# Kernel optimization log

Hardware: AMD Instinct MI355X
Metric: run time of the kernel (lower is better)

Reference implementation:

```python
import jax, jax.numpy as jnp
import numpy as np


def setup_inputs() -> dict:
    key = jax.random.key(0)
    k1, k2, k3, k4 = jax.random.split(key, 4)
    B, n, f, k = 32768, 512, 30, 40
    X = jax.random.normal(k1, (B, n), dtype=jnp.float32)
    w1 = jax.random.normal(k2, (n, 1), dtype=jnp.float32) * 0.01
    b = jnp.zeros((1,), dtype=jnp.float32)
    v = jax.random.normal(k3, (n, f, k), dtype=jnp.float32) * 0.01
    feature2field = jax.random.randint(k4, (n,), 0, f, dtype=jnp.int32)
    return {"X": X, "w1": w1, "b": b, "v": v, "feature2field": feature2field}


def reference(X, w1, b, v, feature2field):
    # linear terms: [B]
    linear = (X @ w1).reshape(-1) + b[0]
    n = v.shape[0]
    # A[i, j] = v[i, feature2field[j]]  -> [n, n, k]
    A = v[:, feature2field, :]
    # pair coefficient C[i, j] = sum_k v[i, field[j], k] * v[j, field[i], k]
    C = jnp.einsum('ijk,jik->ij', A, A)
    # strict upper triangle matches the i<j loop in the original
    Cm = C * jnp.triu(jnp.ones((n, n), dtype=C.dtype), k=1)
    # interaction[b] = sum_{i<j} C[i,j] * X[b,i] * X[b,j]
    inter = jnp.einsum('bi,ij,bj->b', X, Cm, X)
    logits = linear + inter
    return jax.nn.sigmoid(logits)
```

## Files before the change

### kernel.cpp

```cpp
#include <hip/hip_runtime.h>
#include <hip/hip_bf16.h>
#include <math.h>


#define N_FEAT 512
#define FK 1200
#define KDIM 40
#define B_ROWS 32768
#define BM 128
#define BN 128
#define BK 64

typedef __attribute__((ext_vector_type(8))) short short8;
typedef __attribute__((ext_vector_type(4))) float f32x4;

__device__ __forceinline__ unsigned short bf16_rne(float f) {
    union { float f; unsigned int u; } c; c.f = f;
    unsigned int u = c.u;
    u += 0x7fffu + ((u >> 16) & 1u);
    return (unsigned short)(u >> 16);
}

__device__ __forceinline__ void async_copy16(const void* g, void* l) {
    __builtin_amdgcn_global_load_lds(
        (const __attribute__((address_space(1))) void*)g,
        (__attribute__((address_space(3))) void*)l,
        16, 0, 0);
}

__global__ __launch_bounds__(256) void cvt_x(const float* __restrict__ X,
                                             unsigned short* __restrict__ Xb) {
    const int i = blockIdx.x * 256 + threadIdx.x;
    f32x4 x = ((const f32x4*)X)[i];
    ushort4 o;
    o.x = bf16_rne(x.x);
    o.y = bf16_rne(x.y);
    o.z = bf16_rne(x.z);
    o.w = bf16_rne(x.w);
    ((ushort4*)Xb)[i] = o;
}

__global__ __launch_bounds__(256) void build_w16(const float* __restrict__ v,
                                                 const int* __restrict__ f2f,
                                                 unsigned short* __restrict__ W16) {
    const int j = blockIdx.x * 256 + threadIdx.x;
    const int i = blockIdx.y;
    const int fi = f2f[i];
    const int fj = f2f[j];
    const float4* a = (const float4*)(v + (size_t)i * FK + (size_t)fj * KDIM);
    const float4* c = (const float4*)(v + (size_t)j * FK + (size_t)fi * KDIM);
    float acc = 0.f;
#pragma unroll
    for (int q = 0; q < KDIM / 4; ++q) {
        float4 av = a[q], cv = c[q];
        acc = fmaf(av.x, cv.x, acc);
        acc = fmaf(av.y, cv.y, acc);
        acc = fmaf(av.z, cv.z, acc);
        acc = fmaf(av.w, cv.w, acc);
    }
    W16[(size_t)i * N_FEAT + j] = (i == j) ? (unsigned short)0 : bf16_rne(0.5f * acc);
}

__global__ __launch_bounds__(256) void ffm_mfma(const unsigned short* __restrict__ Xb,
                                                const unsigned short* __restrict__ W16,
                                                const float* __restrict__ X,
                                                const float* __restrict__ w1,
                                                float* __restrict__ pOut) {
    __shared__ unsigned short As[BM * BK];
    __shared__ unsigned short Bs[BN * BK];
    __shared__ float part[2][BM];

    const int tid  = threadIdx.x;
    const int lane = tid & 63;
    const int wave = tid >> 6;
    const int wm = wave & 1;
    const int wn = wave >> 1;
    const int quad = lane >> 4;
    const int l16  = lane & 15;

    const int cb   = blockIdx.x;
    const int col0 = cb * BN;
    const size_t row0 = (size_t)blockIdx.y * BM;

    f32x4 acc[4][4];
#pragma unroll
    for (int mi = 0; mi < 4; ++mi)
#pragma unroll
        for (int ni = 0; ni < 4; ++ni)
            acc[mi][ni] = (f32x4){0.f, 0.f, 0.f, 0.f};

    const int srow = lane >> 3;
    const int scol = (((lane & 7) ^ (srow & 7)) * 8);

    const int aswz = l16 & 7;

    for (int k0 = 0; k0 < N_FEAT; k0 += BK) {
#pragma unroll
        for (int c = 0; c < 4; ++c) {
            const int chunk = wave * 4 + c;
            const int r = chunk * 8 + srow;
            async_copy16(Xb  + (row0 + r) * N_FEAT + k0 + scol, As + chunk * 512);
            async_copy16(W16 + (size_t)(col0 + r) * N_FEAT + k0 + scol, Bs + chunk * 512);
        }
        __syncthreads();

#pragma unroll
        for (int kk = 0; kk < 2; ++kk) {
            short8 a[4], b[4];
            const int kc = kk * 4 + quad;
            const int swc = (kc ^ aswz) * 8;
#pragma unroll
            for (int mi = 0; mi < 4; ++mi) {
                const int ar = wm * 64 + mi * 16 + l16;
                a[mi] = *(const short8*)(As + ar * BK + swc);
            }
#pragma unroll
            for (int ni = 0; ni < 4; ++ni) {
                const int br = wn * 64 + ni * 16 + l16;
                b[ni] = *(const short8*)(Bs + br * BK + swc);
            }
#pragma unroll
            for (int mi = 0; mi < 4; ++mi)
#pragma unroll
                for (int ni = 0; ni < 4; ++ni)
                    acc[mi][ni] = __builtin_amdgcn_mfma_f32_16x16x32_bf16(
                        a[mi], b[ni], acc[mi][ni], 0, 0, 0);
        }
        __syncthreads();
    }

#pragma unroll
    for (int mi = 0; mi < 4; ++mi) {
        float rs[4] = {0.f, 0.f, 0.f, 0.f};
        const size_t growb = row0 + wm * 64 + mi * 16 + quad * 4;
#pragma unroll
        for (int ni = 0; ni < 4; ++ni) {
            const int gcol = col0 + wn * 64 + ni * 16 + l16;
            const float w1v = w1[gcol];
#pragma unroll
            for (int reg = 0; reg < 4; ++reg) {
                const float xv = X[(growb + reg) * N_FEAT + gcol];
                rs[reg] += xv * (acc[mi][ni][reg] + w1v);
            }
        }
#pragma unroll
        for (int off = 1; off < 16; off <<= 1)
#pragma unroll
            for (int reg = 0; reg < 4; ++reg)
                rs[reg] += __shfl_xor(rs[reg], off, 16);
        if (l16 == 0) {
            const int lrow = wm * 64 + mi * 16 + quad * 4;
#pragma unroll
            for (int reg = 0; reg < 4; ++reg)
                part[wn][lrow + reg] = rs[reg];
        }
    }
    __syncthreads();

    if (tid < BM) {
        pOut[(size_t)cb * B_ROWS + row0 + tid] = part[0][tid] + part[1][tid];
    }
}

__global__ __launch_bounds__(256) void ffm_final(const float* __restrict__ p,
                                                 const float* __restrict__ bvec,
                                                 float* __restrict__ out) {
    const int i = blockIdx.x * 256 + threadIdx.x;
    const float t = p[i] + p[B_ROWS + i] + p[2 * B_ROWS + i] + p[3 * B_ROWS + i] + bvec[0];
    out[i] = 1.0f / (1.0f + expf(-t));
}

extern "C" void kernel_launch(void* const* d_in, const int* in_sizes, int n_in,
                              void* d_out, int out_size, void* d_ws, size_t ws_size,
                              hipStream_t stream) {
    const float* X   = (const float*)d_in[0];
    const float* w1  = (const float*)d_in[1];
    const float* b   = (const float*)d_in[2];
    const float* v   = (const float*)d_in[3];
    const int*   f2f = (const int*)d_in[4];
    float* out = (float*)d_out;

    unsigned short* W16 = (unsigned short*)d_ws;
    unsigned short* Xb  = (unsigned short*)((char*)d_ws + (1u << 20));
    float*          pP  = (float*)((char*)d_ws + (1u << 20) + (32u << 20));

    cvt_x<<<(B_ROWS * N_FEAT / 4) / 256, 256, 0, stream>>>(X, Xb);
    build_w16<<<dim3(2, N_FEAT), 256, 0, stream>>>(v, f2f, W16);
    ffm_mfma<<<dim3(4, B_ROWS / BM), 256, 0, stream>>>(Xb, W16, X, w1, pP);
    ffm_final<<<B_ROWS / 256, 256, 0, stream>>>(pP, b, out);
}
```

Before: 146.8 us.

## Fuse X conversion, GEMM over all columns, and sigmoid into one kernel

Removes the separate fp32-to-bf16 conversion kernel and the final reduction kernel. Each block now loads its 128 rows of X once, converts them to bf16 and keeps the full 128x512 tile resident in padded LDS. It then loops over all four column blocks of W, forms the X·(W+w1) row dot products in registers, and applies the sigmoid directly. This drops the Xb and partial-sum round trips through global memory and two launches. In exchange the grid shrinks to 256 blocks, and LDS use grows to about 150KB per block, capping occupancy at one block per CU. The epilogue also now uses bf16-rounded X instead of fp32 X, which adds a small accuracy change.

```diff
diff --git a/kernel.cpp b/kernel.cpp
--- a/kernel.cpp
+++ b/kernel.cpp
@@ -8,8 +8,8 @@
 #define KDIM 40
 #define B_ROWS 32768
 #define BM 128
-#define BN 128
 #define BK 64
+#define APAD 520
 
 typedef __attribute__((ext_vector_type(8))) short short8;
 typedef __attribute__((ext_vector_type(4))) float f32x4;
@@ -21,23 +21,17 @@
     return (unsigned short)(u >> 16);
 }
 
+__device__ __forceinline__ float bf16_to_f(unsigned short h) {
+    union { unsigned int u; float f; } c;
+    c.u = ((unsigned int)h) << 16;
+    return c.f;
+}
+
 __device__ __forceinline__ void async_copy16(const void* g, void* l) {
     __builtin_amdgcn_global_load_lds(
         (const __attribute__((address_space(1))) void*)g,
         (__attribute__((address_space(3))) void*)l,
         16, 0, 0);
-}
-
-__global__ __launch_bounds__(256) void cvt_x(const float* __restrict__ X,
-                                             unsigned short* __restrict__ Xb) {
-    const int i = blockIdx.x * 256 + threadIdx.x;
-    f32x4 x = ((const f32x4*)X)[i];
-    ushort4 o;
-    o.x = bf16_rne(x.x);
-    o.y = bf16_rne(x.y);
-    o.z = bf16_rne(x.z);
-    o.w = bf16_rne(x.w);
-    ((ushort4*)Xb)[i] = o;
 }
 
 __global__ __launch_bounds__(256) void build_w16(const float* __restrict__ v,
@@ -61,13 +55,13 @@
     W16[(size_t)i * N_FEAT + j] = (i == j) ? (unsigned short)0 : bf16_rne(0.5f * acc);
 }
 
-__global__ __launch_bounds__(256) void ffm_mfma(const unsigned short* __restrict__ Xb,
-                                                const unsigned short* __restrict__ W16,
-                                                const float* __restrict__ X,
-                                                const float* __restrict__ w1,
-                                                float* __restrict__ pOut) {
-    __shared__ unsigned short As[BM * BK];
-    __shared__ unsigned short Bs[BN * BK];
+__global__ __launch_bounds__(256, 1) void ffm_fused(const float* __restrict__ X,
+                                                    const unsigned short* __restrict__ W16,
+                                                    const float* __restrict__ w1,
+                                                    const float* __restrict__ bvec,
+                                                    float* __restrict__ out) {
+    __shared__ __align__(16) unsigned short As[BM * APAD];
+    __shared__ __align__(16) unsigned short Bs[128 * BK];
     __shared__ float part[2][BM];
 
     const int tid  = threadIdx.x;
@@ -78,96 +72,119 @@
     const int quad = lane >> 4;
     const int l16  = lane & 15;
 
-    const int cb   = blockIdx.x;
-    const int col0 = cb * BN;
-    const size_t row0 = (size_t)blockIdx.y * BM;
-
-    f32x4 acc[4][4];
+    const size_t row0 = (size_t)blockIdx.x * BM;
+
+    {
+        const float4* X4 = (const float4*)(X + row0 * N_FEAT);
+        for (int u = 0; u < 32; ++u) {
+            const int g  = u * 256 + tid;
+            const int r  = g >> 6;
+            const int cc = g & 63;
+            float4 f0 = X4[r * 128 + cc * 2];
+            float4 f1 = X4[r * 128 + cc * 2 + 1];
+            union { unsigned short us[8]; short8 v; } pk;
+            pk.us[0] = bf16_rne(f0.x);
+            pk.us[1] = bf16_rne(f0.y);
+            pk.us[2] = bf16_rne(f0.z);
+            pk.us[3] = bf16_rne(f0.w);
+            pk.us[4] = bf16_rne(f1.x);
+            pk.us[5] = bf16_rne(f1.y);
+            pk.us[6] = bf16_rne(f1.z);
+            pk.us[7] = bf16_rne(f1.w);
+            *(short8*)(As + r * APAD + cc * 8) = pk.v;
+        }
+    }
+
+    const int srow = lane >> 3;
+    const int scol = (((lane & 7) ^ srow) * 8);
+    const int aswz = l16 & 7;
+
+    float rs[4][4];
 #pragma unroll
     for (int mi = 0; mi < 4; ++mi)
 #pragma unroll
+        for (int reg = 0; reg < 4; ++reg) rs[mi][reg] = 0.f;
+
+    for (int cb = 0; cb < 4; ++cb) {
+        const int col0 = cb * 128;
+
+        f32x4 acc[4][4];
+#pragma unroll
+        for (int mi = 0; mi < 4; ++mi)
+#pragma unroll
+            for (int ni = 0; ni < 4; ++ni)
+                acc[mi][ni] = (f32x4){0.f, 0.f, 0.f, 0.f};
+
+        for (int k0 = 0; k0 < N_FEAT; k0 += BK) {
+            __syncthreads();
+#pragma unroll
+            for (int c = 0; c < 4; ++c) {
+                const int chunk = wave * 4 + c;
+                const int r = chunk * 8 + srow;
+                async_copy16(W16 + (size_t)(col0 + r) * N_FEAT + k0 + scol,
+                             Bs + chunk * 512);
+            }
+            __syncthreads();
+
+#pragma unroll
+            for (int kk = 0; kk < 2; ++kk) {
+                short8 a[4], b[4];
+#pragma unroll
+                for (int mi = 0; mi < 4; ++mi) {
+                    const int ar = wm * 64 + mi * 16 + l16;
+                    a[mi] = *(const short8*)(As + ar * APAD + k0 + kk * 32 + quad * 8);
+                }
+                const int swc = ((kk * 4 + quad) ^ aswz) * 8;
+#pragma unroll
+                for (int ni = 0; ni < 4; ++ni) {
+                    const int br = wn * 64 + ni * 16 + l16;
+                    b[ni] = *(const short8*)(Bs + br * BK + swc);
+                }
+#pragma unroll
+                for (int mi = 0; mi < 4; ++mi)
+#pragma unroll
+                    for (int ni = 0; ni < 4; ++ni)
+                        acc[mi][ni] = __builtin_amdgcn_mfma_f32_16x16x32_bf16(
+                            a[mi], b[ni], acc[mi][ni], 0, 0, 0);
+            }
+        }
+
+        float w1v[4];
+#pragma unroll
         for (int ni = 0; ni < 4; ++ni)
-            acc[mi][ni] = (f32x4){0.f, 0.f, 0.f, 0.f};
-
-    const int srow = lane >> 3;
-    const int scol = (((lane & 7) ^ (srow & 7)) * 8);
-
-    const int aswz = l16 & 7;
-
-    for (int k0 = 0; k0 < N_FEAT; k0 += BK) {
-#pragma unroll
-        for (int c = 0; c < 4; ++c) {
-            const int chunk = wave * 4 + c;
-            const int r = chunk * 8 + srow;
-            async_copy16(Xb  + (row0 + r) * N_FEAT + k0 + scol, As + chunk * 512);
-            async_copy16(W16 + (size_t)(col0 + r) * N_FEAT + k0 + scol, Bs + chunk * 512);
-        }
-        __syncthreads();
-
-#pragma unroll
-        for (int kk = 0; kk < 2; ++kk) {
-            short8 a[4], b[4];
-            const int kc = kk * 4 + quad;
-            const int swc = (kc ^ aswz) * 8;
-#pragma unroll
-            for (int mi = 0; mi < 4; ++mi) {
-                const int ar = wm * 64 + mi * 16 + l16;
-                a[mi] = *(const short8*)(As + ar * BK + swc);
+            w1v[ni] = w1[col0 + wn * 64 + ni * 16 + l16];
+#pragma unroll
+        for (int mi = 0; mi < 4; ++mi) {
+#pragma unroll
+            for (int ni = 0; ni < 4; ++ni) {
+                const int gc = col0 + wn * 64 + ni * 16 + l16;
+#pragma unroll
+                for (int reg = 0; reg < 4; ++reg) {
+                    const int row = wm * 64 + mi * 16 + quad * 4 + reg;
+                    const float xf = bf16_to_f(As[row * APAD + gc]);
+                    rs[mi][reg] = fmaf(xf, acc[mi][ni][reg] + w1v[ni], rs[mi][reg]);
+                }
             }
-#pragma unroll
-            for (int ni = 0; ni < 4; ++ni) {
-                const int br = wn * 64 + ni * 16 + l16;
-                b[ni] = *(const short8*)(Bs + br * BK + swc);
-            }
-#pragma unroll
-            for (int mi = 0; mi < 4; ++mi)
-#pragma unroll
-                for (int ni = 0; ni < 4; ++ni)
-                    acc[mi][ni] = __builtin_amdgcn_mfma_f32_16x16x32_bf16(
-                        a[mi], b[ni], acc[mi][ni], 0, 0, 0);
-        }
-        __syncthreads();
-    }
-
-#pragma unroll
-    for (int mi = 0; mi < 4; ++mi) {
-        float rs[4] = {0.f, 0.f, 0.f, 0.f};
-        const size_t growb = row0 + wm * 64 + mi * 16 + quad * 4;
-#pragma unroll
-        for (int ni = 0; ni < 4; ++ni) {
-            const int gcol = col0 + wn * 64 + ni * 16 + l16;
-            const float w1v = w1[gcol];
-#pragma unroll
-            for (int reg = 0; reg < 4; ++reg) {
-                const float xv = X[(growb + reg) * N_FEAT + gcol];
-                rs[reg] += xv * (acc[mi][ni][reg] + w1v);
-            }
-        }
-#pragma unroll
-        for (int off = 1; off < 16; off <<= 1)
-#pragma unroll
-            for (int reg = 0; reg < 4; ++reg)
-                rs[reg] += __shfl_xor(rs[reg], off, 16);
-        if (l16 == 0) {
-            const int lrow = wm * 64 + mi * 16 + quad * 4;
-#pragma unroll
-            for (int reg = 0; reg < 4; ++reg)
-                part[wn][lrow + reg] = rs[reg];
-        }
-    }
+        }
+    }
+
+#pragma unroll
+    for (int mi = 0; mi < 4; ++mi)
+#pragma unroll
+        for (int reg = 0; reg < 4; ++reg) {
+            float r = rs[mi][reg];
+#pragma unroll
+            for (int off = 1; off < 16; off <<= 1)
+                r += __shfl_xor(r, off, 16);
+            if (l16 == 0)
+                part[wn][wm * 64 + mi * 16 + quad * 4 + reg] = r;
+        }
     __syncthreads();
 
     if (tid < BM) {
-        pOut[(size_t)cb * B_ROWS + row0 + tid] = part[0][tid] + part[1][tid];
-    }
-}
-
-__global__ __launch_bounds__(256) void ffm_final(const float* __restrict__ p,
-                                                 const float* __restrict__ bvec,
-                                                 float* __restrict__ out) {
-    const int i = blockIdx.x * 256 + threadIdx.x;
-    const float t = p[i] + p[B_ROWS + i] + p[2 * B_ROWS + i] + p[3 * B_ROWS + i] + bvec[0];
-    out[i] = 1.0f / (1.0f + expf(-t));
+        const float t = part[0][tid] + part[1][tid] + bvec[0];
+        out[row0 + tid] = 1.0f / (1.0f + expf(-t));
+    }
 }
 
 extern "C" void kernel_launch(void* const* d_in, const int* in_sizes, int n_in,
@@ -181,11 +198,7 @@
     float* out = (float*)d_out;
 
     unsigned short* W16 = (unsigned short*)d_ws;
-    unsigned short* Xb  = (unsigned short*)((char*)d_ws + (1u << 20));
-    float*          pP  = (float*)((char*)d_ws + (1u << 20) + (32u << 20));
-
-    cvt_x<<<(B_ROWS * N_FEAT / 4) / 256, 256, 0, stream>>>(X, Xb);
+
     build_w16<<<dim3(2, N_FEAT), 256, 0, stream>>>(v, f2f, W16);
-    ffm_mfma<<<dim3(4, B_ROWS / BM), 256, 0, stream>>>(Xb, W16, X, w1, pP);
-    ffm_final<<<B_ROWS / 256, 256, 0, stream>>>(pP, b, out);
-}
+    ffm_fused<<<B_ROWS / BM, 256, 0, stream>>>(X, W16, w1, b, out);
+}
```

New measurement: 133.9 us. -8.8%, faster.
